# Optimization experiments

Measured on AMD Instinct MI355X. Metric: run time of the kernel, lower is better.

## Reference

```python
import math
import jax, jax.numpy as jnp
import numpy as np

B, T, C = 2, 2048, 1024
NH = 16
HS = C // NH
WIN = 256

def setup_inputs() -> dict:
    key = jax.random.key(0)
    k1, k2, k3 = jax.random.split(key, 3)
    x = jax.random.normal(k1, (B, T, C), dtype=jnp.float32)
    # Linear weights stored as (in, out) so y = x @ W
    scale_attn = 1.0 / math.sqrt(C)
    W_attn = jax.random.normal(k2, (C, 3 * C), dtype=jnp.float32) * scale_attn
    W_proj = jax.random.normal(k3, (C, C), dtype=jnp.float32) * scale_attn
    return {"x": x, "W_attn": W_attn, "W_proj": W_proj}

def reference(x, W_attn, W_proj):
    Bs, Ts, Cs = x.shape
    W = min(WIN, Ts)
    qkv = x @ W_attn                                  # [B,T,3C]
    q, k, v = jnp.split(qkv, 3, axis=-1)
    # [B,T,C] -> [B,NH,T,HS]
    q = q.reshape(Bs, Ts, NH, HS).transpose(0, 2, 1, 3)
    k = k.reshape(Bs, Ts, NH, HS).transpose(0, 2, 1, 3)
    v = v.reshape(Bs, Ts, NH, HS).transpose(0, 2, 1, 3)
    att = jnp.einsum('bhqd,bhkd->bhqk', q, k) * (1.0 / math.sqrt(HS))
    i_idx = jnp.arange(Ts)[:, None]
    j_idx = jnp.arange(Ts)[None, :]
    mask = (j_idx <= i_idx) & (i_idx - j_idx < W)      # causal sliding window
    att = jnp.where(mask[None, None, :, :], att, -jnp.inf)
    att = jax.nn.softmax(att, axis=-1)
    y = jnp.einsum('bhqk,bhkd->bhqd', att, v)          # [B,NH,T,HS]
    y = y.transpose(0, 2, 1, 3).reshape(Bs, Ts, Cs)
    return y @ W_proj
```

## Files before the change

### kernel.cpp

```cpp
#include <hip/hip_runtime.h>
#include <hip/hip_bf16.h>
#include <cstdint>

#define B_   2
#define T_   2048
#define C_   1024
#define NH_  16
#define HS_  64
#define WIN_ 256
#define M_   (B_*T_)

typedef __attribute__((ext_vector_type(8)))  short          short8;
typedef __attribute__((ext_vector_type(8)))  unsigned short ushortx8;
typedef __attribute__((ext_vector_type(8)))  __bf16         bf16x8;
typedef __attribute__((ext_vector_type(4)))  float          floatx4;
typedef __attribute__((ext_vector_type(16))) float          floatx16;

__device__ __forceinline__ unsigned short f2bf(float f) {
    union { float f; uint32_t u; } v; v.f = f;
    uint32_t r = (v.u + 0x7FFFu + ((v.u >> 16) & 1u)) >> 16;
    return (unsigned short)r;
}

__device__ __forceinline__ floatx4 mfma16(short8 a, short8 b, floatx4 c) {
    return __builtin_amdgcn_mfma_f32_16x16x32_bf16(
        __builtin_bit_cast(bf16x8, a), __builtin_bit_cast(bf16x8, b), c, 0, 0, 0);
}
__device__ __forceinline__ floatx16 mfma32(short8 a, short8 b, floatx16 c) {
    return __builtin_amdgcn_mfma_f32_32x32x16_bf16(
        __builtin_bit_cast(bf16x8, a), __builtin_bit_cast(bf16x8, b), c, 0, 0, 0);
}

__device__ __forceinline__ void async16(const void* g, void* l) {
    __builtin_amdgcn_global_load_lds(
        (const __attribute__((address_space(1))) void*)g,
        (__attribute__((address_space(3))) void*)l, 16, 0, 0);
}

#define NB_CONV 4096
#define NB_WA   768
#define NB_WP   256

__device__ void transpose_tile(const float* __restrict__ in, unsigned short* __restrict__ out,
                               int K, int N, int kt, int nt, unsigned short (*tile)[65])
{
    const int k0 = kt * 64, n0 = nt * 64;
    const int tr = threadIdx.x >> 4;
    const int tc = (threadIdx.x & 15) * 4;
    #pragma unroll
    for (int it = 0; it < 4; it++) {
        int row = tr + it * 16;
        float4 v = *(const float4*)&in[(size_t)(k0 + row) * N + n0 + tc];
        tile[row][tc + 0] = f2bf(v.x);
        tile[row][tc + 1] = f2bf(v.y);
        tile[row][tc + 2] = f2bf(v.z);
        tile[row][tc + 3] = f2bf(v.w);
    }
    __syncthreads();
    #pragma unroll
    for (int it = 0; it < 4; it++) {
        int nrow = tr + it * 16;
        ushort4 h;
        h.x = tile[tc + 0][nrow]; h.y = tile[tc + 1][nrow];
        h.z = tile[tc + 2][nrow]; h.w = tile[tc + 3][nrow];
        *(ushort4*)&out[(size_t)(n0 + nrow) * K + k0 + tc] = h;
    }
}

__global__ __launch_bounds__(256)
void prep_kernel(const float* __restrict__ x, const float* __restrict__ W_attn,
                 const float* __restrict__ W_proj,
                 unsigned short* __restrict__ xb, unsigned short* __restrict__ Wa_t,
                 unsigned short* __restrict__ Wp_t)
{
    __shared__ unsigned short tile[64][65];
    const int bid = blockIdx.x;
    if (bid < NB_CONV) {
        int i = (bid * 256 + threadIdx.x) * 4;
        float4 v = *(const float4*)&x[i];
        ushort4 h;
        h.x = f2bf(v.x); h.y = f2bf(v.y); h.z = f2bf(v.z); h.w = f2bf(v.w);
        *(ushort4*)&xb[i] = h;
    } else if (bid < NB_CONV + NB_WA) {
        int idx = bid - NB_CONV;
        transpose_tile(W_attn, Wa_t, C_, 3 * C_, idx / 48, idx % 48, tile);
    } else {
        int idx = bid - NB_CONV - NB_WA;
        transpose_tile(W_proj, Wp_t, C_, C_, idx / 16, idx % 16, tile);
    }
}

template<int MT, bool OUT_BF16, bool VSPLIT>
__global__ __launch_bounds__(256)
void gemm32(const unsigned short* __restrict__ A,
            const unsigned short* __restrict__ Bt,
            void* __restrict__ Cp, unsigned short* __restrict__ vt,
            int M, int N, int K)
{
    constexpr int BK = 64;
    constexpr int BM = 64 * MT;
    __shared__ unsigned short As[BM * BK];
    __shared__ unsigned short Bs[128 * BK];

    const int tid  = threadIdx.x;
    const int lane = tid & 63;
    const int wave = tid >> 6;
    const int l32  = lane & 31;
    const int hi   = lane >> 5;
    const int px   = l32 & 7;
    const int wm   = (wave & 1) * 32 * MT;
    const int wn   = (wave >> 1) * 64;
    const int m0   = blockIdx.y * BM;
    const int n0   = blockIdx.x * 128;

    const int ri = lane >> 3;
    const int pg = lane & 7;
    const int gg = pg ^ ri;

    floatx16 acc[MT][2];
    #pragma unroll
    for (int i = 0; i < MT; i++)
        #pragma unroll
        for (int j = 0; j < 2; j++) acc[i][j] = (floatx16)(0.f);

    const unsigned short* gA = &A[(size_t)(m0 + wave * 8 + ri) * K + gg * 8];
    const unsigned short* gB = &Bt[(size_t)(n0 + wave * 8 + ri) * K + gg * 8];
    unsigned short* lA = &As[(wave * 8) * BK];
    unsigned short* lB = &Bs[(wave * 8) * BK];

    for (int k0 = 0; k0 < K; k0 += BK) {
        #pragma unroll
        for (int s = 0; s < 2 * MT; s++)
            async16(gA + k0 + (size_t)s * 32 * K, lA + s * 32 * BK);
        #pragma unroll
        for (int s = 0; s < 4; s++)
            async16(gB + k0 + (size_t)s * 32 * K, lB + s * 32 * BK);
        __syncthreads();

        #pragma unroll
        for (int ks = 0; ks < 4; ks++) {
            short8 af[MT], bfr[2];
            #pragma unroll
            for (int i = 0; i < MT; i++) {
                int r = wm + i * 32 + l32;
                int p = (ks * 2 + hi) ^ px;
                af[i] = *(const short8*)(&As[r * BK + p * 8]);
            }
            #pragma unroll
            for (int j = 0; j < 2; j++) {
                int r = wn + j * 32 + l32;
                int p = (ks * 2 + hi) ^ px;
                bfr[j] = *(const short8*)(&Bs[r * BK + p * 8]);
            }
            #pragma unroll
            for (int i = 0; i < MT; i++)
                #pragma unroll
                for (int j = 0; j < 2; j++)
                    acc[i][j] = mfma32(af[i], bfr[j], acc[i][j]);
        }
        __syncthreads();
    }

    #pragma unroll
    for (int i = 0; i < MT; i++)
        #pragma unroll
        for (int j = 0; j < 2; j++) {
            const int col  = n0 + wn + j * 32 + l32;
            const int row0 = m0 + wm + i * 32 + 4 * hi;
            if (VSPLIT && col >= 2 * C_) {
                const int hd = col - 2 * C_;
                const int hh = hd >> 6, d = hd & 63;
                #pragma unroll
                for (int g = 0; g < 4; g++) {
                    int rowg = row0 + 8 * g;
                    int bb = rowg >> 11, t = rowg & (T_ - 1);
                    ushort4 h4;
                    h4.x = f2bf(acc[i][j][g * 4 + 0]);
                    h4.y = f2bf(acc[i][j][g * 4 + 1]);
                    h4.z = f2bf(acc[i][j][g * 4 + 2]);
                    h4.w = f2bf(acc[i][j][g * 4 + 3]);
                    *(ushort4*)&vt[((size_t)(bb * NH_ + hh) * 64 + d) * T_ + t] = h4;
                }
            } else {
                #pragma unroll
                for (int g = 0; g < 4; g++)
                    #pragma unroll
                    for (int rr = 0; rr < 4; rr++) {
                        int row = row0 + 8 * g + rr;
                        if (OUT_BF16)
                            ((unsigned short*)Cp)[(size_t)row * N + col] = f2bf(acc[i][j][g * 4 + rr]);
                        else
                            ((float*)Cp)[(size_t)row * N + col] = acc[i][j][g * 4 + rr];
                    }
            }
        }
}

__global__ __launch_bounds__(256)
void attn_kernel(const unsigned short* __restrict__ qkv,
                 const unsigned short* __restrict__ vt,
                 unsigned short* __restrict__ y)
{
    __shared__ unsigned short Ks[64 * 64];
    __shared__ unsigned short Vs[64 * 64];
    __shared__ unsigned short Ps[4][16 * 72];

    const int tid  = threadIdx.x;
    const int lane = tid & 63;
    const int wave = tid >> 6;
    const int l16  = lane & 15;
    const int quad = lane >> 4;
    const int sw   = l16 & 7;

    const int g  = blockIdx.x;
    const int yq = g >> 3;
    const int hb = (g & 7) + 8 * (yq >> 5);
    const int qt = yq & 31;
    const int h  = hb & 15;
    const int b  = hb >> 4;

    const int q0b = qt * 64;
    const int q0w = q0b + wave * 16;
    const size_t base = (size_t)b * T_;
    const int ROW  = 3 * C_;
    const int qoff = h * HS_;
    const int koff = C_ + h * HS_;
    const size_t vbase = ((size_t)(b * NH_ + h) * 64) * T_;
    unsigned short* Pstrip = Ps[wave];
    const float SC = 0.125f * 1.44269504f;

    const int ri = lane >> 3;
    const int gg = (lane & 7) ^ ri;

    short8 aq[2];
    #pragma unroll
    for (int ks = 0; ks < 2; ks++)
        aq[ks] = *(const short8*)&qkv[(base + q0w + l16) * ROW + qoff + ks * 32 + quad * 8];

    floatx4 O[4];
    #pragma unroll
    for (int j = 0; j < 4; j++) O[j] = (floatx4){0.f, 0.f, 0.f, 0.f};
    float psum[4] = {0.f, 0.f, 0.f, 0.f};

    int kb_lo = q0b - (WIN_ - 1);
    kb_lo = (kb_lo > 0 ? kb_lo : 0) & ~63;

    for (int kb = kb_lo; kb <= q0b; kb += 64) {
        __syncthreads();
        #pragma unroll
        for (int c = 0; c < 2; c++) {
            int row = wave * 16 + c * 8;
            async16(&qkv[(base + kb + row + ri) * ROW + koff + gg * 8],
                    &Ks[row * 64]);
            async16(&vt[vbase + (size_t)(row + ri) * T_ + kb + gg * 8],
                    &Vs[row * 64]);
        }
        __syncthreads();

        floatx4 s[4];
        #pragma unroll
        for (int nt = 0; nt < 4; nt++) s[nt] = (floatx4){0.f, 0.f, 0.f, 0.f};
        #pragma unroll
        for (int ks = 0; ks < 2; ks++)
            #pragma unroll
            for (int nt = 0; nt < 4; nt++) {
                short8 bk = *(const short8*)&Ks[(nt * 16 + l16) * 64
                                                + (((ks * 4 + quad) ^ sw) * 8)];
                s[nt] = mfma16(aq[ks], bk, s[nt]);
            }

        #pragma unroll
        for (int nt = 0; nt < 4; nt++)
            #pragma unroll
            for (int r = 0; r < 4; r++) {
                int dist = (q0w + quad * 4 + r) - (kb + nt * 16 + l16);
                float sv = ((unsigned)dist < (unsigned)WIN_) ? s[nt][r] * SC : -1e30f;
                float e = exp2f(sv);
                psum[r] += e;
                s[nt][r] = e;
            }

        #pragma unroll
        for (int nt = 0; nt < 4; nt++)
            #pragma unroll
            for (int r = 0; r < 4; r++)
                Pstrip[(quad * 4 + r) * 72 + nt * 16 + l16] = f2bf(s[nt][r]);

        #pragma unroll
        for (int ks = 0; ks < 2; ks++) {
            short8 ap = *(const short8*)&Pstrip[l16 * 72 + ks * 32 + quad * 8];
            #pragma unroll
            for (int jt = 0; jt < 4; jt++) {
                short8 bv = *(const short8*)&Vs[(jt * 16 + l16) * 64
                                                + (((ks * 4 + quad) ^ sw) * 8)];
                O[jt] = mfma16(ap, bv, O[jt]);
            }
        }
    }

    #pragma unroll
    for (int r = 0; r < 4; r++) {
        #pragma unroll
        for (int off = 8; off >= 1; off >>= 1)
            psum[r] += __shfl_xor(psum[r], off, 64);
    }

    #pragma unroll
    for (int jt = 0; jt < 4; jt++)
        #pragma unroll
        for (int r = 0; r < 4; r++)
            Pstrip[(quad * 4 + r) * 72 + jt * 16 + l16] = f2bf(O[jt][r] / psum[r]);
    #pragma unroll
    for (int it = 0; it < 2; it++) {
        int c = lane + 64 * it;
        int qr = c >> 3, dc = (c & 7) * 8;
        *(ushortx8*)&y[(base + q0w + qr) * C_ + qoff + dc] =
            *(const ushortx8*)&Pstrip[qr * 72 + dc];
    }
}

extern "C" void kernel_launch(void* const* d_in, const int* in_sizes, int n_in,
                              void* d_out, int out_size, void* d_ws, size_t ws_size,
                              hipStream_t stream)
{
    const float* x      = (const float*)d_in[0];
    const float* W_attn = (const float*)d_in[1];
    const float* W_proj = (const float*)d_in[2];
    float* out = (float*)d_out;

    unsigned short* xb   = (unsigned short*)d_ws;
    unsigned short* Wa_t = xb   + (size_t)M_ * C_;
    unsigned short* Wp_t = Wa_t + (size_t)3 * C_ * C_;
    unsigned short* qkv  = Wp_t + (size_t)C_ * C_;
    unsigned short* y    = qkv  + (size_t)M_ * 3 * C_;
    unsigned short* vtg  = y    + (size_t)M_ * C_;

    dim3 blk(256);
    prep_kernel<<<NB_CONV + NB_WA + NB_WP, blk, 0, stream>>>(x, W_attn, W_proj, xb, Wa_t, Wp_t);
    gemm32<2, true, true><<<dim3((3 * C_) / 128, M_ / 128), blk, 0, stream>>>(
        xb, Wa_t, qkv, vtg, M_, 3 * C_, C_);
    attn_kernel<<<(T_ / 64) * NH_ * B_, blk, 0, stream>>>(qkv, vtg, y);
    gemm32<1, false, false><<<dim3(C_ / 128, M_ / 64), blk, 0, stream>>>(
        y, Wp_t, out, nullptr, M_, C_, C_);
}
```

Before: 150.8 us.

## Double-buffer attention K/V tiles, skip interior masking, remap GEMM blocks across XCDs

The attention kernel now double-buffers its K and V shared-memory tiles. It prefetches the next tile with async loads and waits on a partial vmcnt, so global loads overlap with MFMA work. It also skips the window-mask computation for key tiles known to be fully inside the window. Both GEMMs remap the flat block index so that consecutive tiles land on the same XCD (8-way interleave), which is meant to improve L2 reuse. The cost is doubled LDS use in attention and a hand-written waitcnt count that must match the number of async loads issued.

After: 155.3 us. +3.0%, slower.

```diff
diff --git a/kernel.cpp b/kernel.cpp
--- a/kernel.cpp
+++ b/kernel.cpp
@@ -90,7 +90,7 @@
     }
 }
 
-template<int MT, bool OUT_BF16, bool VSPLIT>
+template<int MT, bool OUT_BF16, bool VSPLIT, int GX>
 __global__ __launch_bounds__(256)
 void gemm32(const unsigned short* __restrict__ A,
             const unsigned short* __restrict__ Bt,
@@ -110,8 +110,13 @@
     const int px   = l32 & 7;
     const int wm   = (wave & 1) * 32 * MT;
     const int wn   = (wave >> 1) * 64;
-    const int m0   = blockIdx.y * BM;
-    const int n0   = blockIdx.x * 128;
+
+    const int nwg  = GX * (int)gridDim.y;
+    int gflat = (int)blockIdx.y * GX + (int)blockIdx.x;
+    const int cpx = nwg >> 3;
+    gflat = (gflat & 7) * cpx + (gflat >> 3);
+    const int m0 = (gflat / GX) * BM;
+    const int n0 = (gflat % GX) * 128;
 
     const int ri = lane >> 3;
     const int pg = lane & 7;
@@ -201,8 +206,8 @@
                  const unsigned short* __restrict__ vt,
                  unsigned short* __restrict__ y)
 {
-    __shared__ unsigned short Ks[64 * 64];
-    __shared__ unsigned short Vs[64 * 64];
+    __shared__ unsigned short Ks[2][64 * 64];
+    __shared__ unsigned short Vs[2][64 * 64];
     __shared__ unsigned short Ps[4][16 * 72];
 
     const int tid  = threadIdx.x;
@@ -245,17 +250,35 @@
     int kb_lo = q0b - (WIN_ - 1);
     kb_lo = (kb_lo > 0 ? kb_lo : 0) & ~63;
 
-    for (int kb = kb_lo; kb <= q0b; kb += 64) {
-        __syncthreads();
+    auto stage = [&](int kb, int buf) {
         #pragma unroll
         for (int c = 0; c < 2; c++) {
             int row = wave * 16 + c * 8;
             async16(&qkv[(base + kb + row + ri) * ROW + koff + gg * 8],
-                    &Ks[row * 64]);
+                    &Ks[buf][row * 64]);
             async16(&vt[vbase + (size_t)(row + ri) * T_ + kb + gg * 8],
-                    &Vs[row * 64]);
-        }
-        __syncthreads();
+                    &Vs[buf][row * 64]);
+        }
+    };
+
+    stage(kb_lo, 0);
+    int cur = 0;
+
+    for (int kb = kb_lo; kb <= q0b; kb += 64) {
+        asm volatile("" ::: "memory");
+        __builtin_amdgcn_s_barrier();
+        if (kb < q0b) {
+            stage(kb + 64, cur ^ 1);
+            asm volatile("s_waitcnt vmcnt(4)" ::: "memory");
+        } else {
+            asm volatile("s_waitcnt vmcnt(0)" ::: "memory");
+        }
+        asm volatile("" ::: "memory");
+        __builtin_amdgcn_s_barrier();
+        __builtin_amdgcn_sched_barrier(0);
+
+        const unsigned short* Kc = Ks[cur];
+        const unsigned short* Vc = Vs[cur];
 
         floatx4 s[4];
         #pragma unroll
@@ -264,21 +287,32 @@
         for (int ks = 0; ks < 2; ks++)
             #pragma unroll
             for (int nt = 0; nt < 4; nt++) {
-                short8 bk = *(const short8*)&Ks[(nt * 16 + l16) * 64
+                short8 bk = *(const short8*)&Kc[(nt * 16 + l16) * 64
                                                 + (((ks * 4 + quad) ^ sw) * 8)];
                 s[nt] = mfma16(aq[ks], bk, s[nt]);
             }
 
-        #pragma unroll
-        for (int nt = 0; nt < 4; nt++)
-            #pragma unroll
-            for (int r = 0; r < 4; r++) {
-                int dist = (q0w + quad * 4 + r) - (kb + nt * 16 + l16);
-                float sv = ((unsigned)dist < (unsigned)WIN_) ? s[nt][r] * SC : -1e30f;
-                float e = exp2f(sv);
-                psum[r] += e;
-                s[nt][r] = e;
-            }
+        if (kb != q0b && kb >= q0b - 192) {
+            #pragma unroll
+            for (int nt = 0; nt < 4; nt++)
+                #pragma unroll
+                for (int r = 0; r < 4; r++) {
+                    float e = exp2f(s[nt][r] * SC);
+                    psum[r] += e;
+                    s[nt][r] = e;
+                }
+        } else {
+            #pragma unroll
+            for (int nt = 0; nt < 4; nt++)
+                #pragma unroll
+                for (int r = 0; r < 4; r++) {
+                    int dist = (q0w + quad * 4 + r) - (kb + nt * 16 + l16);
+                    float sv = ((unsigned)dist < (unsigned)WIN_) ? s[nt][r] * SC : -1e30f;
+                    float e = exp2f(sv);
+                    psum[r] += e;
+                    s[nt][r] = e;
+                }
+        }
 
         #pragma unroll
         for (int nt = 0; nt < 4; nt++)
@@ -291,11 +325,12 @@
             short8 ap = *(const short8*)&Pstrip[l16 * 72 + ks * 32 + quad * 8];
             #pragma unroll
             for (int jt = 0; jt < 4; jt++) {
-                short8 bv = *(const short8*)&Vs[(jt * 16 + l16) * 64
+                short8 bv = *(const short8*)&Vc[(jt * 16 + l16) * 64
                                                 + (((ks * 4 + quad) ^ sw) * 8)];
                 O[jt] = mfma16(ap, bv, O[jt]);
             }
         }
+        cur ^= 1;
     }
 
     #pragma unroll
@@ -337,9 +372,9 @@
 
     dim3 blk(256);
     prep_kernel<<<NB_CONV + NB_WA + NB_WP, blk, 0, stream>>>(x, W_attn, W_proj, xb, Wa_t, Wp_t);
-    gemm32<2, true, true><<<dim3((3 * C_) / 128, M_ / 128), blk, 0, stream>>>(
+    gemm32<2, true, true, 24><<<dim3((3 * C_) / 128, M_ / 128), blk, 0, stream>>>(
         xb, Wa_t, qkv, vtg, M_, 3 * C_, C_);
     attn_kernel<<<(T_ / 64) * NH_ * B_, blk, 0, stream>>>(qkv, vtg, y);
-    gemm32<1, false, false><<<dim3(C_ / 128, M_ / 64), blk, 0, stream>>>(
+    gemm32<1, false, false, 8><<<dim3(C_ / 128, M_ / 64), blk, 0, stream>>>(
         y, Wp_t, out, nullptr, M_, C_, C_);
 }
```
